# Kernel tuning notes

Measured on AMD Instinct MI355X. Metric: run time of the kernel, lower is better.

Reference implementation:

```python
import jax, jax.numpy as jnp
import numpy as np
import math

NUM_HEADS = 8
HEAD_DIM = 64
MID = NUM_HEADS * HEAD_DIM  # 512
OUT_FEATURES = 512
NUM_BUCKETS = 32            # rel_pos_num_buckets (module passes 2*this to bucket fn)
MAX_DISTANCE = 128
SCALE = HEAD_DIM ** -0.5


def _relative_position_bucket(rel_pos, num_buckets, max_distance):
    # faithful port of RelativePositionBias._relative_position_bucket
    num_buckets = num_buckets // 2
    ret = (rel_pos >= 0).astype(jnp.int32) * num_buckets
    n = jnp.abs(rel_pos)
    max_exact = max(1, num_buckets // 2)
    denom = math.log(max_distance / max_exact) if max_distance > max_exact else 1.0
    n_float = jnp.maximum(n.astype(jnp.float32), 1.0)
    val_if_large = (max_exact + jnp.log(n_float / max_exact) / denom * (num_buckets - max_exact)).astype(jnp.int32)
    val_if_large = jnp.minimum(val_if_large, num_buckets - 1)
    ret = ret + jnp.where(n < max_exact, n, val_if_large)
    return ret


def rel_pos_bias(table, num_q, num_k):
    # table: [2*NUM_BUCKETS, heads] -> bias [1, heads, q, k]
    q_pos = jnp.arange(num_q, dtype=jnp.int32)
    k_pos = jnp.arange(num_k, dtype=jnp.int32)
    rel = k_pos[None, :] - q_pos[:, None]                      # [q, k]
    bucket = _relative_position_bucket(rel, NUM_BUCKETS * 2, MAX_DISTANCE)
    bias = table[bucket]                                       # [q, k, h]
    return jnp.transpose(bias, (2, 0, 1))[None]                # [1, h, q, k]


def setup_inputs() -> dict:
    key = jax.random.key(0)
    ks = jax.random.split(key, 6)
    b, n = 2, 4096
    q = jax.random.normal(ks[0], (b, n, MID), dtype=jnp.float32)
    k = jax.random.normal(ks[1], (b, n, MID), dtype=jnp.float32)
    v = jax.random.normal(ks[2], (b, n, MID), dtype=jnp.float32)
    # bucket indices range over [0, 2*NUM_BUCKETS); size table accordingly
    rel_bias_table = jax.random.normal(ks[3], (2 * NUM_BUCKETS, NUM_HEADS), dtype=jnp.float32) * 0.02
    W_out = jax.random.normal(ks[4], (MID, OUT_FEATURES), dtype=jnp.float32) * (1.0 / math.sqrt(MID))
    b_out = jax.random.normal(ks[5], (OUT_FEATURES,), dtype=jnp.float32) * 0.01
    return {"q": q, "k": k, "v": v, "rel_bias_table": rel_bias_table, "W_out": W_out, "b_out": b_out}


def reference(q, k, v, rel_bias_table, W_out, b_out):
    b, n, _ = q.shape
    m = k.shape[1]
    split = lambda t: jnp.transpose(t.reshape(t.shape[0], t.shape[1], NUM_HEADS, HEAD_DIM), (0, 2, 1, 3))
    qh, kh, vh = split(q), split(k), split(v)                  # [b, h, n, d]
    sim = jnp.einsum('bhnd,bhmd->bhnm', qh, kh)                # [b, h, n, m]
    sim = sim + rel_pos_bias(rel_bias_table, n, m)             # bias added BEFORE scaling (as in source)
    sim = sim * SCALE
    attn = jax.nn.softmax(sim, axis=-1)
    out = jnp.einsum('bhnm,bhmd->bhnd', attn, vh)              # [b, h, n, d]
    out = jnp.transpose(out, (0, 2, 1, 3)).reshape(b, n, MID)  # [b, n, h*d]
    return out @ W_out + b_out
```

## Files before the change

### kernel.cpp

```cpp
#include <hip/hip_runtime.h>
#include <hip/hip_bf16.h>
#include <math.h>

#define BB 2
#define HH 8
#define NN 4096
#define DD 64
#define MID 512
#define NOUT 512
#define QB 128
#define KVT 64
#define NT (NN / KVT)
#define LOG2E 1.44269504088896340736f
#define SCALE 0.125f

typedef __attribute__((ext_vector_type(8)))  short bf16x8;
typedef __attribute__((ext_vector_type(4)))  float f32x4;
typedef __attribute__((ext_vector_type(16))) float f32x16;

__device__ __forceinline__ short f2bf(float x) {
  unsigned u = __builtin_bit_cast(unsigned, x);
  u = (u + 0x7FFFu + ((u >> 16) & 1u)) >> 16;
  return (short)u;
}

__device__ __forceinline__ int rp_bucket(int rel) {
  int ret = (rel >= 0) ? 32 : 0;
  int n = (rel >= 0) ? rel : -rel;
  if (n < 16) return ret + n;
  float nf = (float)n;
  float vf = 16.0f + (logf(nf * (1.0f / 16.0f)) / 2.0794415416798357f) * 16.0f;
  int vi = (int)vf;
  vi = vi < 31 ? vi : 31;
  return ret + vi;
}

__device__ __forceinline__ unsigned cvtpk(float lo, float hi) {
  unsigned d;
  asm("v_cvt_pk_bf16_f32 %0, %1, %2" : "=v"(d) : "v"(lo), "v"(hi));
  return d;
}

__device__ __forceinline__ void gl2lds16(const void* g, void* l) {
  __builtin_amdgcn_global_load_lds(
      (const __attribute__((address_space(1))) unsigned*)g,
      (__attribute__((address_space(3))) unsigned*)l, 16, 0, 0);
}

__global__ __launch_bounds__(256) void prep_kernel(
    const float* __restrict__ W,  short* __restrict__ Wt,
    const float* __restrict__ K,  short* __restrict__ Kws,
    const float* __restrict__ V,  short* __restrict__ Vtws)
{
  const int bx = blockIdx.x;
  const int t  = threadIdx.x;
  if (bx < 2048) {
    int i = bx * 256 + t;
    int a = i & 7;
    int h = (i >> 3) & 7;
    int n = (i >> 6) & 4095;
    int b = i >> 18;
    const float* src = K + ((size_t)(b * 4096 + n) * 512 + h * 64 + a * 8);
    float4 x0 = *(const float4*)src;
    float4 x1 = *(const float4*)(src + 4);
    union { short s[8]; bf16x8 v; } pk;
    pk.s[0] = f2bf(x0.x); pk.s[1] = f2bf(x0.y); pk.s[2] = f2bf(x0.z); pk.s[3] = f2bf(x0.w);
    pk.s[4] = f2bf(x1.x); pk.s[5] = f2bf(x1.y); pk.s[6] = f2bf(x1.z); pk.s[7] = f2bf(x1.w);
    size_t off = ((size_t)(b * 8 + h) * 4096 + n) * 64 + (size_t)((a ^ (n & 7)) * 8);
    *(bf16x8*)(Kws + off) = pk.v;
  } else if (bx < 3072) {
    __shared__ short Vl[64][72];
    const int idx = bx - 2048;
    const int g = idx & 63;
    const int bh = idx >> 6;
    const int b = bh >> 3, h = bh & 7;
    const int c4 = t & 15, r = t >> 4;
    #pragma unroll
    for (int rr = 0; rr < 4; ++rr) {
      int nl = r + rr * 16;
      const float* src = V + ((size_t)(b * 4096 + g * 64 + nl) * 512 + h * 64 + c4 * 4);
      float4 x = *(const float4*)src;
      Vl[nl][c4 * 4 + 0] = f2bf(x.x);
      Vl[nl][c4 * 4 + 1] = f2bf(x.y);
      Vl[nl][c4 * 4 + 2] = f2bf(x.z);
      Vl[nl][c4 * 4 + 3] = f2bf(x.w);
    }
    __syncthreads();
    #pragma unroll
    for (int it = 0; it < 2; ++it) {
      int u = t + it * 256;
      int d = u >> 3, sp = u & 7;
      int s = sp ^ (d & 7);
      union { short s[8]; bf16x8 v; } pk;
      #pragma unroll
      for (int e = 0; e < 8; ++e) {
        int np  = s * 8 + e;
        int p16 = np & 15;
        int kvl = (np & 48) | (4 * (p16 >> 3) + (p16 & 3) + 8 * ((p16 >> 2) & 1));
        pk.s[e] = Vl[kvl][d];
      }
      *(bf16x8*)(Vtws + ((size_t)bh * 64 + d) * 4096 + g * 64 + sp * 8) = pk.v;
    }
  } else {
    int i = (bx - 3072) * 256 + t;
    int kin = i >> 9, n = i & 511;
    Wt[n * MID + kin] = f2bf(W[i]);
  }
}

__global__ __launch_bounds__(256, 2) void attn_kernel(
    const float* __restrict__ q, const short* __restrict__ kws,
    const short* __restrict__ vtws, const float* __restrict__ table,
    short* __restrict__ attn_out)
{
  __shared__ short Ks[3][4096];
  __shared__ short Vs[3][4096];
  __shared__ float biasb[512];
  __shared__ float Lw[4][32];

  const int tid = threadIdx.x;
  const int w   = tid >> 6;
  const int l   = tid & 63;
  const int lq  = l & 31;
  const int hi  = l >> 5;

  const int raw = blockIdx.x;
  const int bh  = (raw & 7) * 2 + (raw >> 8);
  const int xb  = (raw >> 3) & 31;
  const int b = bh >> 3, h = bh & 7;
  const int q0 = xb * QB;
  const int qw = q0 + w * 32;
  const int qg = qw + lq;

  const float smul = SCALE * LOG2E;

  for (int i = tid; i < 512; i += 256)
    biasb[i] = table[rp_bucket(i - 256) * HH + h] * smul;
  const float c_lo = table[31 * HH + h] * smul;
  const float c_hi = table[63 * HH + h] * smul;

  f32x16 c16h, c16l;
  #pragma unroll
  for (int r = 0; r < 16; ++r) { c16h[r] = c_hi; c16l[r] = c_lo; }

  bf16x8 qf[4];
  {
    const float* qr = q + ((size_t)b * NN + qg) * MID + (size_t)h * DD;
    #pragma unroll
    for (int dc = 0; dc < 4; ++dc) {
      int d0 = dc * 16 + hi * 8;
      float4 a0 = *(const float4*)(qr + d0);
      float4 a1 = *(const float4*)(qr + d0 + 4);
      bf16x8 f;
      f[0] = f2bf(a0.x * smul); f[1] = f2bf(a0.y * smul);
      f[2] = f2bf(a0.z * smul); f[3] = f2bf(a0.w * smul);
      f[4] = f2bf(a1.x * smul); f[5] = f2bf(a1.y * smul);
      f[6] = f2bf(a1.z * smul); f[7] = f2bf(a1.w * smul);
      qf[dc] = f;
    }
  }

  const short* kbh = kws  + (size_t)bh * NN * DD;
  const short* vbh = vtws + (size_t)bh * DD * NN;

  f32x16 o0a = {}, o0b = {}, o1a = {}, o1b = {};
  float ls0 = 0.f, ls1 = 0.f, ls2 = 0.f, ls3 = 0.f;

  const int o1w = w * 1024 + l * 16;
  const int o2w = o1w + 4096;
  const char* pkA = (const char*)kbh + o1w;
  const char* pvA = (const char*)vbh + (size_t)(o1w >> 7) * 8192 + (o1w & 127);
  const char* pvB = (const char*)vbh + (size_t)(o2w >> 7) * 8192 + (o2w & 127);
  char* ldsK = (char*)&Ks[0][0] + w * 1024;
  char* ldsV = (char*)&Vs[0][0] + w * 1024;
  const char* kbase = (const char*)&Ks[0][0];
  const char* vbase = (const char*)&Vs[0][0];

#define STAGE(BOFF) {                                   \
    gl2lds16(pkA,        ldsK + (BOFF));                \
    gl2lds16(pkA + 4096, ldsK + (BOFF) + 4096);         \
    gl2lds16(pvA,        ldsV + (BOFF));                \
    gl2lds16(pvB,        ldsV + (BOFF) + 4096);         \
    pkA += 8192; pvA += 128; pvB += 128; }

  __syncthreads();
  STAGE(0);
  STAGE(8192);

  int bo_cur = 0, bo_nxt = 16384;

  for (int t = 0; t < NT; ++t) {
    if (t + 1 < NT) asm volatile("s_waitcnt vmcnt(4)" ::: "memory");
    else            asm volatile("s_waitcnt vmcnt(0)" ::: "memory");
    __builtin_amdgcn_s_barrier();

    const int kv0 = t * KVT;

    const char* kr0 = kbase + bo_cur + lq * 128;
    const char* kr1 = kr0 + 32 * 128;
    const int swz = lq & 7;
    bf16x8 kf00 = *(const bf16x8*)(kr0 + ((hi ^ swz) << 4));
    bf16x8 kf10 = *(const bf16x8*)(kr1 + ((hi ^ swz) << 4));

    const int lo_rel = kv0 - (qw + 31);
    const int hi_rel = kv0 + KVT - 1 - qw;
    f32x16 acc0, acc1;
    if (lo_rel > 127) {
      acc0 = __builtin_amdgcn_mfma_f32_32x32x16_bf16(kf00, qf[0], c16h, 0, 0, 0);
      acc1 = __builtin_amdgcn_mfma_f32_32x32x16_bf16(kf10, qf[0], c16h, 0, 0, 0);
    } else if (hi_rel < -127) {
      acc0 = __builtin_amdgcn_mfma_f32_32x32x16_bf16(kf00, qf[0], c16l, 0, 0, 0);
      acc1 = __builtin_amdgcn_mfma_f32_32x32x16_bf16(kf10, qf[0], c16l, 0, 0, 0);
    } else {
      const int bidx0 = kv0 - qg + 256;
      f32x16 g0, g1;
      #pragma unroll
      for (int r = 0; r < 16; ++r) {
        int cr = (r & 3) + 8 * (r >> 2) + 4 * hi;
        g0[r] = biasb[bidx0 + cr];
        g1[r] = biasb[bidx0 + 32 + cr];
      }
      acc0 = __builtin_amdgcn_mfma_f32_32x32x16_bf16(kf00, qf[0], g0, 0, 0, 0);
      acc1 = __builtin_amdgcn_mfma_f32_32x32x16_bf16(kf10, qf[0], g1, 0, 0, 0);
    }
    __builtin_amdgcn_s_setprio(1);
    #pragma unroll
    for (int dc = 1; dc < 4; ++dc) {
      bf16x8 kf0 = *(const bf16x8*)(kr0 + (((dc * 2 + hi) ^ swz) << 4));
      bf16x8 kf1 = *(const bf16x8*)(kr1 + (((dc * 2 + hi) ^ swz) << 4));
      acc0 = __builtin_amdgcn_mfma_f32_32x32x16_bf16(kf0, qf[dc], acc0, 0, 0, 0);
      acc1 = __builtin_amdgcn_mfma_f32_32x32x16_bf16(kf1, qf[dc], acc1, 0, 0, 0);
    }
    __builtin_amdgcn_s_setprio(0);

    float p0[16], p1[16];
    #pragma unroll
    for (int r = 0; r < 16; ++r) p0[r] = __builtin_amdgcn_exp2f(acc0[r]);
    #pragma unroll
    for (int r = 0; r < 16; ++r) p1[r] = __builtin_amdgcn_exp2f(acc1[r]);

    ls0 += ((p0[0] + p0[1]) + (p0[2] + p0[3])) + ((p0[4] + p0[5]) + (p0[6] + p0[7]));
    ls1 += ((p0[8] + p0[9]) + (p0[10] + p0[11])) + ((p0[12] + p0[13]) + (p0[14] + p0[15]));
    ls2 += ((p1[0] + p1[1]) + (p1[2] + p1[3])) + ((p1[4] + p1[5]) + (p1[6] + p1[7]));
    ls3 += ((p1[8] + p1[9]) + (p1[10] + p1[11])) + ((p1[12] + p1[13]) + (p1[14] + p1[15]));

    bf16x8 pa[4];
    {
      union { unsigned u[4]; bf16x8 v; } ua, ub, uc, ud;
      ua.u[0] = cvtpk(p0[0],  p0[1]);  ua.u[1] = cvtpk(p0[2],  p0[3]);
      ua.u[2] = cvtpk(p0[4],  p0[5]);  ua.u[3] = cvtpk(p0[6],  p0[7]);
      ub.u[0] = cvtpk(p0[8],  p0[9]);  ub.u[1] = cvtpk(p0[10], p0[11]);
      ub.u[2] = cvtpk(p0[12], p0[13]); ub.u[3] = cvtpk(p0[14], p0[15]);
      uc.u[0] = cvtpk(p1[0],  p1[1]);  uc.u[1] = cvtpk(p1[2],  p1[3]);
      uc.u[2] = cvtpk(p1[4],  p1[5]);  uc.u[3] = cvtpk(p1[6],  p1[7]);
      ud.u[0] = cvtpk(p1[8],  p1[9]);  ud.u[1] = cvtpk(p1[10], p1[11]);
      ud.u[2] = cvtpk(p1[12], p1[13]); ud.u[3] = cvtpk(p1[14], p1[15]);
      pa[0] = ua.v; pa[1] = ub.v; pa[2] = uc.v; pa[3] = ud.v;
    }

    {
      const char* vr0 = vbase + bo_cur + lq * 128;
      const char* vr1 = vr0 + 32 * 128;
      const int s0 = lq & 7;
      __builtin_amdgcn_s_setprio(1);
      #pragma unroll
      for (int ks = 0; ks < 4; ks += 2) {
        bf16x8 vfa0 = *(const bf16x8*)(vr0 + (((hi + 2 * ks) ^ s0) << 4));
        bf16x8 vfb0 = *(const bf16x8*)(vr0 + (((hi + 2 * (ks + 1)) ^ s0) << 4));
        bf16x8 vfa1 = *(const bf16x8*)(vr1 + (((hi + 2 * ks) ^ s0) << 4));
        bf16x8 vfb1 = *(const bf16x8*)(vr1 + (((hi + 2 * (ks + 1)) ^ s0) << 4));
        o0a = __builtin_amdgcn_mfma_f32_32x32x16_bf16(pa[ks],     vfa0, o0a, 0, 0, 0);
        o0b = __builtin_amdgcn_mfma_f32_32x32x16_bf16(pa[ks + 1], vfb0, o0b, 0, 0, 0);
        o1a = __builtin_amdgcn_mfma_f32_32x32x16_bf16(pa[ks],     vfa1, o1a, 0, 0, 0);
        o1b = __builtin_amdgcn_mfma_f32_32x32x16_bf16(pa[ks + 1], vfb1, o1b, 0, 0, 0);
      }
      __builtin_amdgcn_s_setprio(0);
    }

    if (t + 2 < NT) STAGE(bo_nxt);
    bo_cur = (bo_cur == 16384) ? 0 : bo_cur + 8192;
    bo_nxt = (bo_nxt == 16384) ? 0 : bo_nxt + 8192;
  }

  f32x16 o0, o1;
  #pragma unroll
  for (int r = 0; r < 16; ++r) { o0[r] = o0a[r] + o0b[r]; o1[r] = o1a[r] + o1b[r]; }
  float lsum = (ls0 + ls1) + (ls2 + ls3);
  float tot = lsum + __shfl_xor(lsum, 32);
  if (l < 32) Lw[w][l] = tot;
  __syncthreads();
  float inv[16];
  #pragma unroll
  for (int g = 0; g < 4; ++g) {
    f32x4 t4 = *(const f32x4*)&Lw[w][g * 8 + hi * 4];
    inv[g * 4 + 0] = 1.0f / t4[0];
    inv[g * 4 + 1] = 1.0f / t4[1];
    inv[g * 4 + 2] = 1.0f / t4[2];
    inv[g * 4 + 3] = 1.0f / t4[3];
  }
  const size_t ob = ((size_t)b * NN + qw) * MID + (size_t)h * DD;
  #pragma unroll
  for (int r = 0; r < 16; ++r) {
    const int crow = (r & 3) + 8 * (r >> 2) + 4 * hi;
    short* orow = attn_out + ob + (size_t)crow * MID;
    orow[lq]      = f2bf(o0[r] * inv[r]);
    orow[32 + lq] = f2bf(o1[r] * inv[r]);
  }
#undef STAGE
}

__global__ __launch_bounds__(256) void proj_kernel(
    const short* __restrict__ A, const short* __restrict__ Wt,
    const float* __restrict__ bias, float* __restrict__ out)
{
  const int tid = threadIdx.x;
  const int w  = tid >> 6;
  const int l  = tid & 63;
  const int lr = l & 15;
  const int lg = l >> 4;
  const int m0 = blockIdx.x * 64 + w * 16;
  const int n0 = blockIdx.y * 64;

  f32x4 acc[4] = {};
  const short* ar = A + (size_t)(m0 + lr) * MID + lg * 8;
  #pragma unroll
  for (int kk = 0; kk < MID; kk += 32) {
    bf16x8 af = *(const bf16x8*)(ar + kk);
    #pragma unroll
    for (int u = 0; u < 4; ++u) {
      bf16x8 bfr = *(const bf16x8*)(Wt + (size_t)(n0 + u * 16 + lr) * MID + kk + lg * 8);
      acc[u] = __builtin_amdgcn_mfma_f32_16x16x32_bf16(af, bfr, acc[u], 0, 0, 0);
    }
  }
  #pragma unroll
  for (int u = 0; u < 4; ++u) {
    float bb = bias[n0 + u * 16 + lr];
    #pragma unroll
    for (int r = 0; r < 4; ++r)
      out[(size_t)(m0 + lg * 4 + r) * NOUT + n0 + u * 16 + lr] = acc[u][r] + bb;
  }
}

extern "C" void kernel_launch(void* const* d_in, const int* in_sizes, int n_in,
                              void* d_out, int out_size, void* d_ws, size_t ws_size,
                              hipStream_t stream) {
  const float* q     = (const float*)d_in[0];
  const float* k     = (const float*)d_in[1];
  const float* v     = (const float*)d_in[2];
  const float* table = (const float*)d_in[3];
  const float* W     = (const float*)d_in[4];
  const float* bo    = (const float*)d_in[5];
  float* out = (float*)d_out;

  char* wsp = (char*)d_ws;
  short* attn_ws = (short*)wsp;                       wsp += (size_t)BB * NN * MID * 2;
  short* Wt      = (short*)wsp;                       wsp += (size_t)MID * NOUT * 2;
  short* kws     = (short*)wsp;                       wsp += (size_t)BB * HH * NN * DD * 2;
  short* vtws    = (short*)wsp;

  hipLaunchKernelGGL(prep_kernel, dim3(4096), dim3(256), 0, stream,
                     W, Wt, k, kws, v, vtws);
  hipLaunchKernelGGL(attn_kernel, dim3(BB * HH * (NN / QB)), dim3(256), 0, stream,
                     q, kws, vtws, table, attn_ws);
  hipLaunchKernelGGL(proj_kernel, dim3(BB * NN / 64, NOUT / 64), dim3(256), 0, stream,
                     attn_ws, Wt, bo, out);
}
```

Baseline: 132.7 us.

## Deepen KV pipeline to four LDS stages, unroll loop, tile W transpose

The attention kernel's K/V staging ring grows from three to four LDS buffers, keeping three tiles in flight. The main loop is unrolled by four so buffer offsets and vmcnt wait counts become compile-time constants. The prep kernel now uses packed bf16 conversion for K and V, and transposes W through LDS in 64x64 tiles instead of doing strided scalar stores, which cuts its grid to 3136 blocks. LDS per block grows from about 50KB to about 66KB, so two blocks per CU may no longer fit, and the unrolled body raises code size and register pressure.

New measurement: 270.7 us. +104.0%, slower.

```diff
diff --git a/kernel.cpp b/kernel.cpp
--- a/kernel.cpp
+++ b/kernel.cpp
@@ -63,9 +63,9 @@
     const float* src = K + ((size_t)(b * 4096 + n) * 512 + h * 64 + a * 8);
     float4 x0 = *(const float4*)src;
     float4 x1 = *(const float4*)(src + 4);
-    union { short s[8]; bf16x8 v; } pk;
-    pk.s[0] = f2bf(x0.x); pk.s[1] = f2bf(x0.y); pk.s[2] = f2bf(x0.z); pk.s[3] = f2bf(x0.w);
-    pk.s[4] = f2bf(x1.x); pk.s[5] = f2bf(x1.y); pk.s[6] = f2bf(x1.z); pk.s[7] = f2bf(x1.w);
+    union { unsigned u[4]; bf16x8 v; } pk;
+    pk.u[0] = cvtpk(x0.x, x0.y); pk.u[1] = cvtpk(x0.z, x0.w);
+    pk.u[2] = cvtpk(x1.x, x1.y); pk.u[3] = cvtpk(x1.z, x1.w);
     size_t off = ((size_t)(b * 8 + h) * 4096 + n) * 64 + (size_t)((a ^ (n & 7)) * 8);
     *(bf16x8*)(Kws + off) = pk.v;
   } else if (bx < 3072) {
@@ -80,10 +80,9 @@
       int nl = r + rr * 16;
       const float* src = V + ((size_t)(b * 4096 + g * 64 + nl) * 512 + h * 64 + c4 * 4);
       float4 x = *(const float4*)src;
-      Vl[nl][c4 * 4 + 0] = f2bf(x.x);
-      Vl[nl][c4 * 4 + 1] = f2bf(x.y);
-      Vl[nl][c4 * 4 + 2] = f2bf(x.z);
-      Vl[nl][c4 * 4 + 3] = f2bf(x.w);
+      unsigned lo = cvtpk(x.x, x.y), hi2 = cvtpk(x.z, x.w);
+      unsigned* dst = (unsigned*)&Vl[nl][c4 * 4];
+      dst[0] = lo; dst[1] = hi2;
     }
     __syncthreads();
     #pragma unroll
@@ -102,19 +101,43 @@
       *(bf16x8*)(Vtws + ((size_t)bh * 64 + d) * 4096 + g * 64 + sp * 8) = pk.v;
     }
   } else {
-    int i = (bx - 3072) * 256 + t;
-    int kin = i >> 9, n = i & 511;
-    Wt[n * MID + kin] = f2bf(W[i]);
-  }
-}
+    __shared__ short Wl[64][72];
+    const int idx = bx - 3072;
+    const int k0 = (idx & 7) * 64;
+    const int n0 = (idx >> 3) * 64;
+    const int c4 = t & 15, r = t >> 4;
+    #pragma unroll
+    for (int rr = 0; rr < 4; ++rr) {
+      int kl = r + rr * 16;
+      const float* src = W + (size_t)(k0 + kl) * 512 + n0 + c4 * 4;
+      float4 x = *(const float4*)src;
+      unsigned lo = cvtpk(x.x, x.y), hi2 = cvtpk(x.z, x.w);
+      unsigned* dst = (unsigned*)&Wl[kl][c4 * 4];
+      dst[0] = lo; dst[1] = hi2;
+    }
+    __syncthreads();
+    #pragma unroll
+    for (int it = 0; it < 2; ++it) {
+      int u = t + it * 256;
+      int nl = u >> 3, a = u & 7;
+      union { short s[8]; bf16x8 v; } pk;
+      #pragma unroll
+      for (int e = 0; e < 8; ++e) pk.s[e] = Wl[a * 8 + e][nl];
+      *(bf16x8*)(Wt + (size_t)(n0 + nl) * 512 + k0 + a * 8) = pk.v;
+    }
+  }
+}
+
+#define VMW_(N) asm volatile("s_waitcnt vmcnt(" #N ")" ::: "memory")
+#define VMW(N) VMW_(N)
 
 __global__ __launch_bounds__(256, 2) void attn_kernel(
     const float* __restrict__ q, const short* __restrict__ kws,
     const short* __restrict__ vtws, const float* __restrict__ table,
     short* __restrict__ attn_out)
 {
-  __shared__ short Ks[3][4096];
-  __shared__ short Vs[3][4096];
+  __shared__ short Ks[4][4096];
+  __shared__ short Vs[4][4096];
   __shared__ float biasb[512];
   __shared__ float Lw[4][32];
 
@@ -173,8 +196,12 @@
   const char* pvB = (const char*)vbh + (size_t)(o2w >> 7) * 8192 + (o2w & 127);
   char* ldsK = (char*)&Ks[0][0] + w * 1024;
   char* ldsV = (char*)&Vs[0][0] + w * 1024;
-  const char* kbase = (const char*)&Ks[0][0];
-  const char* vbase = (const char*)&Vs[0][0];
+
+  const char* kr0b = (const char*)&Ks[0][0] + lq * 128;
+  const char* kr1b = kr0b + 32 * 128;
+  const char* vr0b = (const char*)&Vs[0][0] + lq * 128;
+  const char* vr1b = vr0b + 32 * 128;
+  const int swz = lq & 7;
 
 #define STAGE(BOFF) {                                   \
     gl2lds16(pkA,        ldsK + (BOFF));                \
@@ -183,104 +210,100 @@
     gl2lds16(pvB,        ldsV + (BOFF) + 4096);         \
     pkA += 8192; pvA += 128; pvB += 128; }
 
+#define BODY(T, BOFF, VMLIT) {                                               \
+    VMW(VMLIT);                                                              \
+    __builtin_amdgcn_s_barrier();                                            \
+    const int kv0 = (T) * KVT;                                               \
+    const char* kr0 = kr0b + (BOFF);                                         \
+    const char* kr1 = kr1b + (BOFF);                                         \
+    bf16x8 kf00 = *(const bf16x8*)(kr0 + ((hi ^ swz) << 4));                 \
+    bf16x8 kf10 = *(const bf16x8*)(kr1 + ((hi ^ swz) << 4));                 \
+    const int lo_rel = kv0 - (qw + 31);                                      \
+    const int hi_rel = kv0 + KVT - 1 - qw;                                   \
+    f32x16 acc0, acc1;                                                       \
+    if (lo_rel > 127) {                                                      \
+      acc0 = __builtin_amdgcn_mfma_f32_32x32x16_bf16(kf00, qf[0], c16h, 0, 0, 0); \
+      acc1 = __builtin_amdgcn_mfma_f32_32x32x16_bf16(kf10, qf[0], c16h, 0, 0, 0); \
+    } else if (hi_rel < -127) {                                              \
+      acc0 = __builtin_amdgcn_mfma_f32_32x32x16_bf16(kf00, qf[0], c16l, 0, 0, 0); \
+      acc1 = __builtin_amdgcn_mfma_f32_32x32x16_bf16(kf10, qf[0], c16l, 0, 0, 0); \
+    } else {                                                                 \
+      const int bidx0 = kv0 - qg + 256;                                      \
+      f32x16 g0, g1;                                                         \
+      _Pragma("unroll")                                                      \
+      for (int r = 0; r < 16; ++r) {                                         \
+        int cr = (r & 3) + 8 * (r >> 2) + 4 * hi;                            \
+        g0[r] = biasb[bidx0 + cr];                                           \
+        g1[r] = biasb[bidx0 + 32 + cr];                                      \
+      }                                                                      \
+      acc0 = __builtin_amdgcn_mfma_f32_32x32x16_bf16(kf00, qf[0], g0, 0, 0, 0); \
+      acc1 = __builtin_amdgcn_mfma_f32_32x32x16_bf16(kf10, qf[0], g1, 0, 0, 0); \
+    }                                                                        \
+    __builtin_amdgcn_s_setprio(1);                                           \
+    _Pragma("unroll")                                                        \
+    for (int dc = 1; dc < 4; ++dc) {                                         \
+      bf16x8 kf0 = *(const bf16x8*)(kr0 + (((dc * 2 + hi) ^ swz) << 4));     \
+      bf16x8 kf1 = *(const bf16x8*)(kr1 + (((dc * 2 + hi) ^ swz) << 4));     \
+      acc0 = __builtin_amdgcn_mfma_f32_32x32x16_bf16(kf0, qf[dc], acc0, 0, 0, 0); \
+      acc1 = __builtin_amdgcn_mfma_f32_32x32x16_bf16(kf1, qf[dc], acc1, 0, 0, 0); \
+    }                                                                        \
+    __builtin_amdgcn_s_setprio(0);                                           \
+    float p0[16], p1[16];                                                    \
+    _Pragma("unroll")                                                        \
+    for (int r = 0; r < 16; ++r) p0[r] = __builtin_amdgcn_exp2f(acc0[r]);    \
+    _Pragma("unroll")                                                        \
+    for (int r = 0; r < 16; ++r) p1[r] = __builtin_amdgcn_exp2f(acc1[r]);    \
+    ls0 += ((p0[0] + p0[1]) + (p0[2] + p0[3])) + ((p0[4] + p0[5]) + (p0[6] + p0[7]));     \
+    ls1 += ((p0[8] + p0[9]) + (p0[10] + p0[11])) + ((p0[12] + p0[13]) + (p0[14] + p0[15])); \
+    ls2 += ((p1[0] + p1[1]) + (p1[2] + p1[3])) + ((p1[4] + p1[5]) + (p1[6] + p1[7]));     \
+    ls3 += ((p1[8] + p1[9]) + (p1[10] + p1[11])) + ((p1[12] + p1[13]) + (p1[14] + p1[15])); \
+    bf16x8 pa[4];                                                            \
+    {                                                                        \
+      union { unsigned u[4]; bf16x8 v; } ua, ub, uc, ud;                     \
+      ua.u[0] = cvtpk(p0[0],  p0[1]);  ua.u[1] = cvtpk(p0[2],  p0[3]);       \
+      ua.u[2] = cvtpk(p0[4],  p0[5]);  ua.u[3] = cvtpk(p0[6],  p0[7]);       \
+      ub.u[0] = cvtpk(p0[8],  p0[9]);  ub.u[1] = cvtpk(p0[10], p0[11]);      \
+      ub.u[2] = cvtpk(p0[12], p0[13]); ub.u[3] = cvtpk(p0[14], p0[15]);      \
+      uc.u[0] = cvtpk(p1[0],  p1[1]);  uc.u[1] = cvtpk(p1[2],  p1[3]);       \
+      uc.u[2] = cvtpk(p1[4],  p1[5]);  uc.u[3] = cvtpk(p1[6],  p1[7]);       \
+      ud.u[0] = cvtpk(p1[8],  p1[9]);  ud.u[1] = cvtpk(p1[10], p1[11]);      \
+      ud.u[2] = cvtpk(p1[12], p1[13]); ud.u[3] = cvtpk(p1[14], p1[15]);      \
+      pa[0] = ua.v; pa[1] = ub.v; pa[2] = uc.v; pa[3] = ud.v;                \
+    }                                                                        \
+    {                                                                        \
+      const char* vr0 = vr0b + (BOFF);                                       \
+      const char* vr1 = vr1b + (BOFF);                                       \
+      __builtin_amdgcn_s_setprio(1);                                         \
+      _Pragma("unroll")                                                      \
+      for (int ks = 0; ks < 4; ks += 2) {                                    \
+        bf16x8 vfa0 = *(const bf16x8*)(vr0 + (((hi + 2 * ks) ^ swz) << 4));  \
+        bf16x8 vfb0 = *(const bf16x8*)(vr0 + (((hi + 2 * (ks + 1)) ^ swz) << 4)); \
+        bf16x8 vfa1 = *(const bf16x8*)(vr1 + (((hi + 2 * ks) ^ swz) << 4));  \
+        bf16x8 vfb1 = *(const bf16x8*)(vr1 + (((hi + 2 * (ks + 1)) ^ swz) << 4)); \
+        o0a = __builtin_amdgcn_mfma_f32_32x32x16_bf16(pa[ks],     vfa0, o0a, 0, 0, 0); \
+        o0b = __builtin_amdgcn_mfma_f32_32x32x16_bf16(pa[ks + 1], vfb0, o0b, 0, 0, 0); \
+        o1a = __builtin_amdgcn_mfma_f32_32x32x16_bf16(pa[ks],     vfa1, o1a, 0, 0, 0); \
+        o1b = __builtin_amdgcn_mfma_f32_32x32x16_bf16(pa[ks + 1], vfb1, o1b, 0, 0, 0); \
+      }                                                                      \
+      __builtin_amdgcn_s_setprio(0);                                         \
+    }                                                                        \
+    if ((T) + 3 < NT) STAGE((((BOFF) + 24576) & 32767)); }
+
   __syncthreads();
   STAGE(0);
   STAGE(8192);
-
-  int bo_cur = 0, bo_nxt = 16384;
-
-  for (int t = 0; t < NT; ++t) {
-    if (t + 1 < NT) asm volatile("s_waitcnt vmcnt(4)" ::: "memory");
-    else            asm volatile("s_waitcnt vmcnt(0)" ::: "memory");
-    __builtin_amdgcn_s_barrier();
-
-    const int kv0 = t * KVT;
-
-    const char* kr0 = kbase + bo_cur + lq * 128;
-    const char* kr1 = kr0 + 32 * 128;
-    const int swz = lq & 7;
-    bf16x8 kf00 = *(const bf16x8*)(kr0 + ((hi ^ swz) << 4));
-    bf16x8 kf10 = *(const bf16x8*)(kr1 + ((hi ^ swz) << 4));
-
-    const int lo_rel = kv0 - (qw + 31);
-    const int hi_rel = kv0 + KVT - 1 - qw;
-    f32x16 acc0, acc1;
-    if (lo_rel > 127) {
-      acc0 = __builtin_amdgcn_mfma_f32_32x32x16_bf16(kf00, qf[0], c16h, 0, 0, 0);
-      acc1 = __builtin_amdgcn_mfma_f32_32x32x16_bf16(kf10, qf[0], c16h, 0, 0, 0);
-    } else if (hi_rel < -127) {
-      acc0 = __builtin_amdgcn_mfma_f32_32x32x16_bf16(kf00, qf[0], c16l, 0, 0, 0);
-      acc1 = __builtin_amdgcn_mfma_f32_32x32x16_bf16(kf10, qf[0], c16l, 0, 0, 0);
-    } else {
-      const int bidx0 = kv0 - qg + 256;
-      f32x16 g0, g1;
-      #pragma unroll
-      for (int r = 0; r < 16; ++r) {
-        int cr = (r & 3) + 8 * (r >> 2) + 4 * hi;
-        g0[r] = biasb[bidx0 + cr];
-        g1[r] = biasb[bidx0 + 32 + cr];
-      }
-      acc0 = __builtin_amdgcn_mfma_f32_32x32x16_bf16(kf00, qf[0], g0, 0, 0, 0);
-      acc1 = __builtin_amdgcn_mfma_f32_32x32x16_bf16(kf10, qf[0], g1, 0, 0, 0);
-    }
-    __builtin_amdgcn_s_setprio(1);
-    #pragma unroll
-    for (int dc = 1; dc < 4; ++dc) {
-      bf16x8 kf0 = *(const bf16x8*)(kr0 + (((dc * 2 + hi) ^ swz) << 4));
-      bf16x8 kf1 = *(const bf16x8*)(kr1 + (((dc * 2 + hi) ^ swz) << 4));
-      acc0 = __builtin_amdgcn_mfma_f32_32x32x16_bf16(kf0, qf[dc], acc0, 0, 0, 0);
-      acc1 = __builtin_amdgcn_mfma_f32_32x32x16_bf16(kf1, qf[dc], acc1, 0, 0, 0);
-    }
-    __builtin_amdgcn_s_setprio(0);
-
-    float p0[16], p1[16];
-    #pragma unroll
-    for (int r = 0; r < 16; ++r) p0[r] = __builtin_amdgcn_exp2f(acc0[r]);
-    #pragma unroll
-    for (int r = 0; r < 16; ++r) p1[r] = __builtin_amdgcn_exp2f(acc1[r]);
-
-    ls0 += ((p0[0] + p0[1]) + (p0[2] + p0[3])) + ((p0[4] + p0[5]) + (p0[6] + p0[7]));
-    ls1 += ((p0[8] + p0[9]) + (p0[10] + p0[11])) + ((p0[12] + p0[13]) + (p0[14] + p0[15]));
-    ls2 += ((p1[0] + p1[1]) + (p1[2] + p1[3])) + ((p1[4] + p1[5]) + (p1[6] + p1[7]));
-    ls3 += ((p1[8] + p1[9]) + (p1[10] + p1[11])) + ((p1[12] + p1[13]) + (p1[14] + p1[15]));
-
-    bf16x8 pa[4];
-    {
-      union { unsigned u[4]; bf16x8 v; } ua, ub, uc, ud;
-      ua.u[0] = cvtpk(p0[0],  p0[1]);  ua.u[1] = cvtpk(p0[2],  p0[3]);
-      ua.u[2] = cvtpk(p0[4],  p0[5]);  ua.u[3] = cvtpk(p0[6],  p0[7]);
-      ub.u[0] = cvtpk(p0[8],  p0[9]);  ub.u[1] = cvtpk(p0[10], p0[11]);
-      ub.u[2] = cvtpk(p0[12], p0[13]); ub.u[3] = cvtpk(p0[14], p0[15]);
-      uc.u[0] = cvtpk(p1[0],  p1[1]);  uc.u[1] = cvtpk(p1[2],  p1[3]);
-      uc.u[2] = cvtpk(p1[4],  p1[5]);  uc.u[3] = cvtpk(p1[6],  p1[7]);
-      ud.u[0] = cvtpk(p1[8],  p1[9]);  ud.u[1] = cvtpk(p1[10], p1[11]);
-      ud.u[2] = cvtpk(p1[12], p1[13]); ud.u[3] = cvtpk(p1[14], p1[15]);
-      pa[0] = ua.v; pa[1] = ub.v; pa[2] = uc.v; pa[3] = ud.v;
-    }
-
-    {
-      const char* vr0 = vbase + bo_cur + lq * 128;
-      const char* vr1 = vr0 + 32 * 128;
-      const int s0 = lq & 7;
-      __builtin_amdgcn_s_setprio(1);
-      #pragma unroll
-      for (int ks = 0; ks < 4; ks += 2) {
-        bf16x8 vfa0 = *(const bf16x8*)(vr0 + (((hi + 2 * ks) ^ s0) << 4));
-        bf16x8 vfb0 = *(const bf16x8*)(vr0 + (((hi + 2 * (ks + 1)) ^ s0) << 4));
-        bf16x8 vfa1 = *(const bf16x8*)(vr1 + (((hi + 2 * ks) ^ s0) << 4));
-        bf16x8 vfb1 = *(const bf16x8*)(vr1 + (((hi + 2 * (ks + 1)) ^ s0) << 4));
-        o0a = __builtin_amdgcn_mfma_f32_32x32x16_bf16(pa[ks],     vfa0, o0a, 0, 0, 0);
-        o0b = __builtin_amdgcn_mfma_f32_32x32x16_bf16(pa[ks + 1], vfb0, o0b, 0, 0, 0);
-        o1a = __builtin_amdgcn_mfma_f32_32x32x16_bf16(pa[ks],     vfa1, o1a, 0, 0, 0);
-        o1b = __builtin_amdgcn_mfma_f32_32x32x16_bf16(pa[ks + 1], vfb1, o1b, 0, 0, 0);
-      }
-      __builtin_amdgcn_s_setprio(0);
-    }
-
-    if (t + 2 < NT) STAGE(bo_nxt);
-    bo_cur = (bo_cur == 16384) ? 0 : bo_cur + 8192;
-    bo_nxt = (bo_nxt == 16384) ? 0 : bo_nxt + 8192;
-  }
+  STAGE(16384);
+
+  for (int tt = 0; tt < NT - 4; tt += 4) {
+    BODY(tt + 0, 0,     8);
+    BODY(tt + 1, 8192,  8);
+    BODY(tt + 2, 16384, 8);
+    BODY(tt + 3, 24576, 8);
+  }
+  BODY(NT - 4, 0,     8);
+  BODY(NT - 3, 8192,  8);
+  BODY(NT - 2, 16384, 4);
+  BODY(NT - 1, 24576, 0);
 
   f32x16 o0, o1;
   #pragma unroll
@@ -307,6 +330,7 @@
     orow[32 + lq] = f2bf(o1[r] * inv[r]);
   }
 #undef STAGE
+#undef BODY
 }
 
 __global__ __launch_bounds__(256) void proj_kernel(
@@ -358,7 +382,7 @@
   short* kws     = (short*)wsp;                       wsp += (size_t)BB * HH * NN * DD * 2;
   short* vtws    = (short*)wsp;
 
-  hipLaunchKernelGGL(prep_kernel, dim3(4096), dim3(256), 0, stream,
+  hipLaunchKernelGGL(prep_kernel, dim3(3136), dim3(256), 0, stream,
                      W, Wt, k, kws, v, vtws);
   hipLaunchKernelGGL(attn_kernel, dim3(BB * HH * (NN / QB)), dim3(256), 0, stream,
                      q, kws, vtws, table, attn_ws);
```
